# Kernel optimization log

Measured on AMD Instinct MI355X. Metric: run time of the kernel, lower is better.

## Reference

```python
import jax, jax.numpy as jnp
import numpy as np

E = 8            # n_expert
K = 2            # n_expert_per_token
C = 2048         # n_embd
I = 1408         # moe_intermediate_size
IS = I * 2       # shared expert intermediate (n_shared_expert=2)
B, T = 2, 2048


def setup_inputs() -> dict:
    key = jax.random.key(0)
    ks = jax.random.split(key, 9)
    s = 0.02
    return {
        "x": jax.random.normal(ks[0], (B, T, C), dtype=jnp.float32),
        "gate_w": jax.random.normal(ks[1], (E, C), dtype=jnp.float32) * s,
        # expert MLP weights, torch Linear convention (out_features, in_features)
        "w1": jax.random.normal(ks[2], (E, I, C), dtype=jnp.float32) * s,  # fc_1
        "w2": jax.random.normal(ks[3], (E, I, C), dtype=jnp.float32) * s,  # fc_2
        "w3": jax.random.normal(ks[4], (E, C, I), dtype=jnp.float32) * s,  # proj
        # shared expert
        "sw1": jax.random.normal(ks[5], (IS, C), dtype=jnp.float32) * s,
        "sw2": jax.random.normal(ks[6], (IS, C), dtype=jnp.float32) * s,
        "sw3": jax.random.normal(ks[7], (C, IS), dtype=jnp.float32) * s,
    }


def reference(x, gate_w, w1, w2, w3, sw1, sw2, sw3):
    Bq, Tq, Cq = x.shape
    xf = x.reshape(-1, Cq)  # [N, C], N = B*T

    # top-k routing: softmax in fp32, then top-k probs per token
    logits = xf @ gate_w.T                                   # [N, E]
    probs = jax.nn.softmax(logits.astype(jnp.float32), axis=-1)
    topk_p, topk_i = jax.lax.top_k(probs, K)                 # [N, K]
    # combine weights: comb[n, e] = sum_k topk_p[n,k] * (topk_i[n,k] == e)
    comb = (jax.nn.one_hot(topk_i, E, dtype=jnp.float32)
            * topk_p[..., None]).sum(axis=1).astype(x.dtype)  # [N, E]

    # per-expert gated-SiLU MLP (batched over experts via einsum)
    h1 = jnp.einsum('nc,eic->eni', xf, w1)                   # [E, N, I]
    h2 = jnp.einsum('nc,eic->eni', xf, w2)                   # [E, N, I]
    h = jax.nn.silu(h1) * h2
    eo = jnp.einsum('eni,eci->enc', h, w3)                   # [E, N, C]

    # weighted scatter-combine
    y = jnp.einsum('enc,ne->nc', eo, comb).reshape(Bq, Tq, Cq)

    # shared expert on the residual input
    sh = (jax.nn.silu(xf @ sw1.T) * (xf @ sw2.T)) @ sw3.T    # [N, C]
    return y + sh.reshape(Bq, Tq, Cq)
```

## Files before the change

### kernel.cpp

```cpp
#include <hip/hip_runtime.h>
#include <stdint.h>

#define N_TOK 4096
#define CDIM  2048
#define NEXP  8
#define IDIM  1408
#define ISDIM 2816
#define CAP   2048
#define ICAT  2816
#define SCAT  5632

typedef __attribute__((ext_vector_type(8))) short bf16x8;
typedef __attribute__((ext_vector_type(4))) float f32x4;

#define GLOAD16(gp, lp) __builtin_amdgcn_global_load_lds( \
    (const __attribute__((address_space(1))) void*)(gp),  \
    (__attribute__((address_space(3))) void*)(lp), 16, 0, 0)

__device__ __forceinline__ unsigned short f2bf(float f) {
  union { float f; unsigned u; } c; c.f = f;
  return (unsigned short)((c.u + 0x7FFFu + ((c.u >> 16) & 1u)) >> 16);
}
__device__ __forceinline__ float bf2f(unsigned short h) {
  union { unsigned u; float f; } c; c.u = (unsigned)h << 16;
  return c.f;
}

__global__ __launch_bounds__(256) void cvt_all(
    const float* __restrict__ x, const float* __restrict__ w1,
    const float* __restrict__ w2, const float* __restrict__ w3,
    const float* __restrict__ sw1, const float* __restrict__ sw2,
    const float* __restrict__ sw3,
    unsigned short* __restrict__ xb, unsigned short* __restrict__ wcat,
    unsigned short* __restrict__ w3b, unsigned short* __restrict__ swcat,
    unsigned short* __restrict__ sw3b) {
  const int b = blockIdx.x;
  const int t = threadIdx.x;
  const float* src;
  unsigned short* dst;
  if (b < 4096) {
    src = x + (size_t)b * 2048;  dst = xb + (size_t)b * 2048;
  } else if (b < 15360) {
    size_t o = (size_t)(b - 4096) * 2048;  src = w3 + o;  dst = w3b + o;
  } else if (b < 18176) {
    size_t o = (size_t)(b - 15360) * 2048; src = sw3 + o; dst = sw3b + o;
  } else if (b < 40704) {
    int g = b - 18176;
    int e = g / 2816, r = g - e * 2816;
    int dr;
    if (r < 1408) { src = w1 + ((size_t)e * 1408 + r) * 2048; dr = (r >> 7) * 256 + (r & 127); }
    else { int r2 = r - 1408; src = w2 + ((size_t)e * 1408 + r2) * 2048; dr = (r2 >> 7) * 256 + 128 + (r2 & 127); }
    dst = wcat + ((size_t)e * ICAT + dr) * 2048;
  } else {
    int g = b - 40704;
    int dr;
    if (g < 2816) {
      int zn = g >= 1408, rr = g - zn * 1408;
      src = sw1 + (size_t)g * 2048;
      dr = zn * 2816 + (rr >> 7) * 256 + (rr & 127);
    } else {
      int r = g - 2816;
      int zn = r >= 1408, rr = r - zn * 1408;
      src = sw2 + (size_t)r * 2048;
      dr = zn * 2816 + (rr >> 7) * 256 + 128 + (rr & 127);
    }
    dst = swcat + (size_t)dr * 2048;
  }
  size_t i = (size_t)t * 8;
  float4 v0 = *(const float4*)(src + i);
  float4 v1 = *(const float4*)(src + i + 4);
  bf16x8 o;
  o[0] = (short)f2bf(v0.x); o[1] = (short)f2bf(v0.y);
  o[2] = (short)f2bf(v0.z); o[3] = (short)f2bf(v0.w);
  o[4] = (short)f2bf(v1.x); o[5] = (short)f2bf(v1.y);
  o[6] = (short)f2bf(v1.z); o[7] = (short)f2bf(v1.w);
  *(bf16x8*)(dst + i) = o;
}

__global__ __launch_bounds__(64) void routing_kernel(
    const float* __restrict__ x, const float* __restrict__ gw,
    int* __restrict__ counts, int* __restrict__ list,
    int* __restrict__ slot_of, float* __restrict__ wts) {
  const int n = blockIdx.x;
  const int lane = threadIdx.x;
  const float* xr = x + (size_t)n * CDIM;
  float s[NEXP];
#pragma unroll
  for (int e = 0; e < NEXP; e++) s[e] = 0.f;
  for (int c = lane; c < CDIM; c += 64) {
    float xv = xr[c];
#pragma unroll
    for (int e = 0; e < NEXP; e++) s[e] += xv * gw[e * CDIM + c];
  }
#pragma unroll
  for (int e = 0; e < NEXP; e++) {
    float v = s[e];
    for (int o = 32; o > 0; o >>= 1) v += __shfl_down(v, o);
    s[e] = v;
  }
  if (lane == 0) {
    float mx = s[0];
#pragma unroll
    for (int e = 1; e < NEXP; e++) mx = fmaxf(mx, s[e]);
    float p[NEXP], sum = 0.f;
#pragma unroll
    for (int e = 0; e < NEXP; e++) { p[e] = __expf(s[e] - mx); sum += p[e]; }
    int i0 = 0;
#pragma unroll
    for (int e = 1; e < NEXP; e++) if (p[e] > p[i0]) i0 = e;
    int i1 = (i0 == 0) ? 1 : 0;
#pragma unroll
    for (int e = 0; e < NEXP; e++) if (e != i0 && p[e] > p[i1]) i1 = e;
    float inv = 1.f / sum;
    int s0 = atomicAdd(&counts[i0], 1);
    int s1 = atomicAdd(&counts[i1], 1);
    if (s0 < CAP) list[i0 * CAP + s0] = n; else s0 = 0;
    if (s1 < CAP) list[i1 * CAP + s1] = n; else s1 = 0;
    slot_of[n * 2]     = i0 * CAP + s0;
    slot_of[n * 2 + 1] = i1 * CAP + s1;
    wts[n * 2]     = p[i0] * inv;
    wts[n * 2 + 1] = p[i1] * inv;
  }
}

template <int PHASE>
__global__ __launch_bounds__(512) void moe_gemm(
    const unsigned short* __restrict__ xb,
    const unsigned short* __restrict__ swcat,
    const unsigned short* __restrict__ wcat,
    unsigned short* __restrict__ hs_out,
    unsigned short* __restrict__ he_out,
    const unsigned short* __restrict__ hs,
    const unsigned short* __restrict__ sw3b,
    const unsigned short* __restrict__ he,
    const unsigned short* __restrict__ w3b,
    float* __restrict__ ysf,
    unsigned short* __restrict__ eo,
    const int* __restrict__ list,
    const int* __restrict__ counts,
    int* __restrict__ ctr) {
  __shared__ __align__(16) char lds[3][32768];
  __shared__ int s_w;

  const int tid = threadIdx.x;
  const int srow = tid >> 2;
  const int c16  = (tid & 3) << 4;
  const int scol = c16 ^ (((srow >> 1) & 3) << 4);
  const int lane = tid & 63, wid = tid >> 6;
  const int wr = wid >> 2, wc = wid & 3;
  const int lrow = lane & 15;
  const int klane = (lane >> 4) << 4;
  const int rsw = ((lrow >> 1) & 3) << 4;
  const int aOff = (wr * 128 + lrow) * 64 + (klane ^ rsw);
  const int bOff = 16384 + (wc * 64 + lrow) * 64 + (klane ^ rsw);
  const int r4 = (lane >> 4) * 4;
  const int TOT = (PHASE == 1) ? 12 * 88 : 10 * 64;

  for (;;) {
    if (tid == 0) s_w = atomicAdd(ctr, 1);
    __syncthreads();
    const int w = s_w;
    if (w >= TOT) break;
    int z, mt, nt;
    if (PHASE == 1) { z = w / 88; int r = w - z * 88; mt = r & 7; nt = r >> 3; }
    else            { z = w / 64; int r = w - z * 64; mt = r & 7; nt = r >> 3; }

    const unsigned short *A, *B;
    unsigned short* O = nullptr;
    float* Of = nullptr;
    int Ka, ldo;
    int cnt = 1 << 30;
    const int* lst = nullptr;
    bool gath = false;
    if (PHASE == 1) {
      Ka = CDIM;
      if (z < 4) {
        int zm = z >> 1, zn = z & 1;
        A = xb + (size_t)zm * 2048 * CDIM;
        B = swcat + (size_t)zn * 2816 * CDIM;
        O = hs_out + (size_t)zm * 2048 * ISDIM + (size_t)zn * 1408;
        ldo = ISDIM;
      } else {
        int e = z - 4;
        cnt = counts[e]; if (cnt > CAP) cnt = CAP;
        lst = list + e * CAP;
        gath = true;
        A = xb;
        B = wcat + (size_t)e * ICAT * CDIM;
        O = he_out + (size_t)e * CAP * IDIM;
        ldo = IDIM;
      }
    } else {
      if (z < 2) {
        Ka = ISDIM;
        A = hs + (size_t)z * 2048 * ISDIM;
        B = sw3b;
        Of = ysf + (size_t)z * 2048 * CDIM;
        ldo = CDIM;
      } else {
        int e = z - 2;
        cnt = counts[e]; if (cnt > CAP) cnt = CAP;
        Ka = IDIM;
        A = he + (size_t)e * CAP * IDIM;
        B = w3b + (size_t)e * CDIM * IDIM;
        O = eo + (size_t)e * CAP * CDIM;
        ldo = CDIM;
      }
    }
    if (mt * 256 >= cnt) continue;

    const char *aS0, *aS1, *bS0, *bS1;
    {
      int ar0 = mt * 256 + srow;
      int ar1 = mt * 256 + 128 + srow;
      if (PHASE == 1 && gath) {
        ar0 = (ar0 < cnt) ? lst[ar0] : lst[0];
        ar1 = (ar1 < cnt) ? lst[ar1] : lst[0];
      }
      aS0 = (const char*)A + (size_t)ar0 * Ka * 2 + scol;
      aS1 = (const char*)A + (size_t)ar1 * Ka * 2 + scol;
      bS0 = (const char*)B + (size_t)(nt * 256 + srow) * Ka * 2 + scol;
      bS1 = (const char*)B + (size_t)(nt * 256 + 128 + srow) * Ka * 2 + scol;
    }
    auto stage = [&](int buf, int kt) {
      size_t kb = (size_t)kt * 64;
      char* d = &lds[buf][0] + tid * 16;
      GLOAD16(aS0 + kb, d);
      GLOAD16(aS1 + kb, d + 8192);
      GLOAD16(bS0 + kb, d + 16384);
      GLOAD16(bS1 + kb, d + 24576);
    };

    f32x4 acc[8][4];
#pragma unroll
    for (int mf = 0; mf < 8; mf++)
#pragma unroll
      for (int nf = 0; nf < 4; nf++) acc[mf][nf] = (f32x4){0.f, 0.f, 0.f, 0.f};

    stage(0, 0);
    stage(1, 1);

    const int ntk = Ka >> 5;
    int cur = 0, nx2 = 2;
    for (int t = 0; t < ntk; t++) {
      if (t + 1 < ntk) asm volatile("s_waitcnt vmcnt(4)" ::: "memory");
      else             asm volatile("s_waitcnt vmcnt(0)" ::: "memory");
      __builtin_amdgcn_s_barrier();
      const char* base = lds[cur];
      bf16x8 aR[8], bR[4];
#pragma unroll
      for (int i = 0; i < 8; i++) aR[i] = *(const bf16x8*)(base + aOff + i * 1024);
#pragma unroll
      for (int i = 0; i < 4; i++) bR[i] = *(const bf16x8*)(base + bOff + i * 1024);
      if (t + 2 < ntk) stage(nx2, t + 2);
      __builtin_amdgcn_s_setprio(1);
#pragma unroll
      for (int nf = 0; nf < 4; nf++)
#pragma unroll
        for (int mf = 0; mf < 8; mf++)
          acc[mf][nf] = __builtin_amdgcn_mfma_f32_16x16x32_bf16(
              aR[mf], bR[nf], acc[mf][nf], 0, 0, 0);
      __builtin_amdgcn_s_setprio(0);
      cur = (cur == 2) ? 0 : cur + 1;
      nx2 = (nx2 == 2) ? 0 : nx2 + 1;
    }

    if (PHASE == 1) {
      __syncthreads();
      unsigned short* ldsH = (unsigned short*)&lds[0][0];
      if (wc >= 2) {
        const int cb = (wc - 2) * 64;
#pragma unroll
        for (int mf = 0; mf < 8; mf++)
#pragma unroll
          for (int nf = 0; nf < 4; nf++) {
            int cc = cb + nf * 16 + lrow;
#pragma unroll
            for (int r = 0; r < 4; r++) {
              int rr = wr * 128 + mf * 16 + r4 + r;
              ldsH[rr * 128 + (cc ^ (((rr >> 2) & 7) << 4))] = f2bf(acc[mf][nf][r]);
            }
          }
      }
      __syncthreads();
      if (wc < 2) {
        const int cb = wc * 64;
#pragma unroll
        for (int mf = 0; mf < 8; mf++) {
#pragma unroll
          for (int nf = 0; nf < 4; nf++) {
            int cc = cb + nf * 16 + lrow;
            int col = nt * 128 + cc;
#pragma unroll
            for (int r = 0; r < 4; r++) {
              int rr = wr * 128 + mf * 16 + r4 + r;
              float z1 = acc[mf][nf][r];
              float z2 = bf2f(ldsH[rr * 128 + (cc ^ (((rr >> 2) & 7) << 4))]);
              float gv = z1 / (1.f + __expf(-z1)) * z2;
              O[(size_t)(mt * 256 + rr) * ldo + col] = f2bf(gv);
            }
          }
        }
      }
      __syncthreads();
    } else {
      const int rowb = mt * 256 + wr * 128;
      const int colb = nt * 256 + wc * 64;
#pragma unroll
      for (int mf = 0; mf < 8; mf++) {
        int row0 = rowb + mf * 16 + r4;
#pragma unroll
        for (int nf = 0; nf < 4; nf++) {
          int col = colb + nf * 16 + lrow;
#pragma unroll
          for (int r = 0; r < 4; r++) {
            if (z < 2)
              Of[(size_t)(row0 + r) * ldo + col] = acc[mf][nf][r];
            else
              O[(size_t)(row0 + r) * ldo + col] = f2bf(acc[mf][nf][r]);
          }
        }
      }
    }
  }
}

__global__ __launch_bounds__(256) void combine_kernel(
    float* __restrict__ y, const float* __restrict__ ysf,
    const unsigned short* __restrict__ eo,
    const int* __restrict__ slot_of, const float* __restrict__ wts) {
  int idx = blockIdx.x * 256 + threadIdx.x;
  int n = idx >> 9;
  int c = (idx & 511) * 4;
  float4 v = *(const float4*)(ysf + (size_t)n * CDIM + c);
#pragma unroll
  for (int k = 0; k < 2; k++) {
    int slot = slot_of[n * 2 + k];
    float w = wts[n * 2 + k];
    ushort4 h = *(const ushort4*)(eo + (size_t)slot * CDIM + c);
    v.x += w * bf2f(h.x);
    v.y += w * bf2f(h.y);
    v.z += w * bf2f(h.z);
    v.w += w * bf2f(h.w);
  }
  *(float4*)(y + (size_t)n * CDIM + c) = v;
}

extern "C" void kernel_launch(void* const* d_in, const int* in_sizes, int n_in,
                              void* d_out, int out_size, void* d_ws, size_t ws_size,
                              hipStream_t stream) {
  const float* x   = (const float*)d_in[0];
  const float* gw  = (const float*)d_in[1];
  const float* w1  = (const float*)d_in[2];
  const float* w2  = (const float*)d_in[3];
  const float* w3  = (const float*)d_in[4];
  const float* sw1 = (const float*)d_in[5];
  const float* sw2 = (const float*)d_in[6];
  const float* sw3 = (const float*)d_in[7];
  float* y = (float*)d_out;

  char* ws = (char*)d_ws;
  size_t off = 0;
  auto alloc = [&](size_t b) -> void* {
    void* p = ws + off;
    off += (b + 255) & ~(size_t)255;
    return p;
  };
  unsigned short* xb    = (unsigned short*)alloc((size_t)N_TOK * CDIM * 2);
  unsigned short* wcat  = (unsigned short*)alloc((size_t)NEXP * ICAT * CDIM * 2);
  unsigned short* w3b   = (unsigned short*)alloc((size_t)NEXP * CDIM * IDIM * 2);
  unsigned short* swcat = (unsigned short*)alloc((size_t)SCAT * CDIM * 2);
  unsigned short* sw3b  = (unsigned short*)alloc((size_t)CDIM * ISDIM * 2);
  unsigned short* hs    = (unsigned short*)alloc((size_t)N_TOK * ISDIM * 2);
  unsigned short* he    = (unsigned short*)alloc((size_t)NEXP * CAP * IDIM * 2);
  float*          ysf   = (float*)alloc((size_t)N_TOK * CDIM * 4);
  int*   counts  = (int*)alloc(NEXP * 4);
  int*   list    = (int*)alloc((size_t)NEXP * CAP * 4);
  int*   slot_of = (int*)alloc((size_t)N_TOK * 2 * 4);
  float* wtsb    = (float*)alloc((size_t)N_TOK * 2 * 4);
  int*   ctrs    = (int*)alloc(2 * 4);
  unsigned short* eoB = wcat;

  hipMemsetAsync(counts, 0, NEXP * 4, stream);
  hipMemsetAsync(ctrs, 0, 2 * 4, stream);
  routing_kernel<<<N_TOK, 64, 0, stream>>>(x, gw, counts, list, slot_of, wtsb);

  cvt_all<<<46336, 256, 0, stream>>>(x, w1, w2, w3, sw1, sw2, sw3,
                                     xb, wcat, w3b, swcat, sw3b);

  moe_gemm<1><<<dim3(256, 1, 1), 512, 0, stream>>>(
      xb, swcat, wcat, hs, he, hs, sw3b, he, w3b, ysf, eoB, list, counts, ctrs + 0);

  moe_gemm<2><<<dim3(256, 1, 1), 512, 0, stream>>>(
      xb, swcat, wcat, hs, he, hs, sw3b, he, w3b, ysf, eoB, list, counts, ctrs + 1);

  combine_kernel<<<(N_TOK * (CDIM / 4)) / 256, 256, 0, stream>>>(y, ysf, eoB, slot_of, wtsb);
}
```

Measured before the change: 596.0 us.

## Split shared-expert down-projection K dimension into two tiles with separate partial outputs

The shared-expert down-projection in phase 2 is split along its K dimension into two halves of 1408, doubling its tile count so the work items resemble the per-expert tiles (K=1408) and the persistent work queue balances better. Each half writes its own fp32 partial buffer, and the combine kernel sums the two partials. This adds an extra 32 MB fp32 buffer write and read in exchange for shorter, more even tail work in the GEMM.

```diff
diff --git a/kernel.cpp b/kernel.cpp
--- a/kernel.cpp
+++ b/kernel.cpp
@@ -134,7 +134,8 @@
     const unsigned short* __restrict__ sw3b,
     const unsigned short* __restrict__ he,
     const unsigned short* __restrict__ w3b,
-    float* __restrict__ ysf,
+    float* __restrict__ ysf0,
+    float* __restrict__ ysf1,
     unsigned short* __restrict__ eo,
     const int* __restrict__ list,
     const int* __restrict__ counts,
@@ -154,7 +155,7 @@
   const int aOff = (wr * 128 + lrow) * 64 + (klane ^ rsw);
   const int bOff = 16384 + (wc * 64 + lrow) * 64 + (klane ^ rsw);
   const int r4 = (lane >> 4) * 4;
-  const int TOT = (PHASE == 1) ? 12 * 88 : 10 * 64;
+  const int TOT = (PHASE == 1) ? 12 * 88 : 12 * 64;
 
   for (;;) {
     if (tid == 0) s_w = atomicAdd(ctr, 1);
@@ -163,17 +164,17 @@
     if (w >= TOT) break;
     int z, mt, nt;
     if (PHASE == 1) { z = w / 88; int r = w - z * 88; mt = r & 7; nt = r >> 3; }
-    else            { z = w / 64; int r = w - z * 64; mt = r & 7; nt = r >> 3; }
+    else            { z = w >> 6; int r = w & 63;     mt = r & 7; nt = r >> 3; }
 
     const unsigned short *A, *B;
     unsigned short* O = nullptr;
     float* Of = nullptr;
-    int Ka, ldo;
+    int Ka, lda, ldb, ldo;
     int cnt = 1 << 30;
     const int* lst = nullptr;
     bool gath = false;
     if (PHASE == 1) {
-      Ka = CDIM;
+      Ka = CDIM; lda = CDIM; ldb = CDIM;
       if (z < 4) {
         int zm = z >> 1, zn = z & 1;
         A = xb + (size_t)zm * 2048 * CDIM;
@@ -191,16 +192,18 @@
         ldo = IDIM;
       }
     } else {
-      if (z < 2) {
-        Ka = ISDIM;
-        A = hs + (size_t)z * 2048 * ISDIM;
-        B = sw3b;
-        Of = ysf + (size_t)z * 2048 * CDIM;
+      Ka = 1408;
+      if (z < 4) {
+        int zm = z >> 1, kh = z & 1;
+        lda = ISDIM; ldb = ISDIM;
+        A = hs + (size_t)zm * 2048 * ISDIM + (size_t)kh * 1408;
+        B = sw3b + (size_t)kh * 1408;
+        Of = (kh ? ysf1 : ysf0) + (size_t)zm * 2048 * CDIM;
         ldo = CDIM;
       } else {
-        int e = z - 2;
+        int e = z - 4;
         cnt = counts[e]; if (cnt > CAP) cnt = CAP;
-        Ka = IDIM;
+        lda = IDIM; ldb = IDIM;
         A = he + (size_t)e * CAP * IDIM;
         B = w3b + (size_t)e * CDIM * IDIM;
         O = eo + (size_t)e * CAP * CDIM;
@@ -217,10 +220,10 @@
         ar0 = (ar0 < cnt) ? lst[ar0] : lst[0];
         ar1 = (ar1 < cnt) ? lst[ar1] : lst[0];
       }
-      aS0 = (const char*)A + (size_t)ar0 * Ka * 2 + scol;
-      aS1 = (const char*)A + (size_t)ar1 * Ka * 2 + scol;
-      bS0 = (const char*)B + (size_t)(nt * 256 + srow) * Ka * 2 + scol;
-      bS1 = (const char*)B + (size_t)(nt * 256 + 128 + srow) * Ka * 2 + scol;
+      aS0 = (const char*)A + (size_t)ar0 * lda * 2 + scol;
+      aS1 = (const char*)A + (size_t)ar1 * lda * 2 + scol;
+      bS0 = (const char*)B + (size_t)(nt * 256 + srow) * ldb * 2 + scol;
+      bS1 = (const char*)B + (size_t)(nt * 256 + 128 + srow) * ldb * 2 + scol;
     }
     auto stage = [&](int buf, int kt) {
       size_t kb = (size_t)kt * 64;
@@ -314,7 +317,7 @@
           int col = colb + nf * 16 + lrow;
 #pragma unroll
           for (int r = 0; r < 4; r++) {
-            if (z < 2)
+            if (z < 4)
               Of[(size_t)(row0 + r) * ldo + col] = acc[mf][nf][r];
             else
               O[(size_t)(row0 + r) * ldo + col] = f2bf(acc[mf][nf][r]);
@@ -326,13 +329,16 @@
 }
 
 __global__ __launch_bounds__(256) void combine_kernel(
-    float* __restrict__ y, const float* __restrict__ ysf,
+    float* __restrict__ y, const float* __restrict__ ysf0,
+    const float* __restrict__ ysf1,
     const unsigned short* __restrict__ eo,
     const int* __restrict__ slot_of, const float* __restrict__ wts) {
   int idx = blockIdx.x * 256 + threadIdx.x;
   int n = idx >> 9;
   int c = (idx & 511) * 4;
-  float4 v = *(const float4*)(ysf + (size_t)n * CDIM + c);
+  float4 v = *(const float4*)(ysf0 + (size_t)n * CDIM + c);
+  float4 v1 = *(const float4*)(ysf1 + (size_t)n * CDIM + c);
+  v.x += v1.x; v.y += v1.y; v.z += v1.z; v.w += v1.w;
 #pragma unroll
   for (int k = 0; k < 2; k++) {
     int slot = slot_of[n * 2 + k];
@@ -373,7 +379,8 @@
   unsigned short* sw3b  = (unsigned short*)alloc((size_t)CDIM * ISDIM * 2);
   unsigned short* hs    = (unsigned short*)alloc((size_t)N_TOK * ISDIM * 2);
   unsigned short* he    = (unsigned short*)alloc((size_t)NEXP * CAP * IDIM * 2);
-  float*          ysf   = (float*)alloc((size_t)N_TOK * CDIM * 4);
+  float*          ysf0  = (float*)alloc((size_t)N_TOK * CDIM * 4);
+  float*          ysf1  = (float*)alloc((size_t)N_TOK * CDIM * 4);
   int*   counts  = (int*)alloc(NEXP * 4);
   int*   list    = (int*)alloc((size_t)NEXP * CAP * 4);
   int*   slot_of = (int*)alloc((size_t)N_TOK * 2 * 4);
@@ -389,10 +396,13 @@
                                      xb, wcat, w3b, swcat, sw3b);
 
   moe_gemm<1><<<dim3(256, 1, 1), 512, 0, stream>>>(
-      xb, swcat, wcat, hs, he, hs, sw3b, he, w3b, ysf, eoB, list, counts, ctrs + 0);
+      xb, swcat, wcat, hs, he, hs, sw3b, he, w3b, ysf0, ysf1, eoB,
+      list, counts, ctrs + 0);
 
   moe_gemm<2><<<dim3(256, 1, 1), 512, 0, stream>>>(
-      xb, swcat, wcat, hs, he, hs, sw3b, he, w3b, ysf, eoB, list, counts, ctrs + 1);
-
-  combine_kernel<<<(N_TOK * (CDIM / 4)) / 256, 256, 0, stream>>>(y, ysf, eoB, slot_of, wtsb);
-}
+      xb, swcat, wcat, hs, he, hs, sw3b, he, w3b, ysf0, ysf1, eoB,
+      list, counts, ctrs + 1);
+
+  combine_kernel<<<(N_TOK * (CDIM / 4)) / 256, 256, 0, stream>>>(
+      y, ysf0, ysf1, eoB, slot_of, wtsb);
+}
```

Result: slower. 618.7 us (+3.8%).

## Partition GEMM work queue into per-XCD panel segments for cache locality

Applied to the files above, without the earlier changes.

Replaces the single global atomic work counter with eight per-segment counters. Each block starts on the segment selected by its blockIdx modulo 8 and steals from the other segments once its own is drained. Panels (z, nt) are interleaved across segments so that blocks on the same XCD tend to process all M-tiles of one weight panel, with the intent of reusing B tiles in that XCD's L2. Costs include extra counters and the possibility of contention or imbalance toward the end of the work.

```diff
diff --git a/kernel.cpp b/kernel.cpp
--- a/kernel.cpp
+++ b/kernel.cpp
@@ -154,170 +154,176 @@
   const int aOff = (wr * 128 + lrow) * 64 + (klane ^ rsw);
   const int bOff = 16384 + (wc * 64 + lrow) * 64 + (klane ^ rsw);
   const int r4 = (lane >> 4) * 4;
-  const int TOT = (PHASE == 1) ? 12 * 88 : 10 * 64;
-
-  for (;;) {
-    if (tid == 0) s_w = atomicAdd(ctr, 1);
-    __syncthreads();
-    const int w = s_w;
-    if (w >= TOT) break;
-    int z, mt, nt;
-    if (PHASE == 1) { z = w / 88; int r = w - z * 88; mt = r & 7; nt = r >> 3; }
-    else            { z = w / 64; int r = w - z * 64; mt = r & 7; nt = r >> 3; }
-
-    const unsigned short *A, *B;
-    unsigned short* O = nullptr;
-    float* Of = nullptr;
-    int Ka, ldo;
-    int cnt = 1 << 30;
-    const int* lst = nullptr;
-    bool gath = false;
-    if (PHASE == 1) {
-      Ka = CDIM;
-      if (z < 4) {
-        int zm = z >> 1, zn = z & 1;
-        A = xb + (size_t)zm * 2048 * CDIM;
-        B = swcat + (size_t)zn * 2816 * CDIM;
-        O = hs_out + (size_t)zm * 2048 * ISDIM + (size_t)zn * 1408;
-        ldo = ISDIM;
+  const int NPAN = (PHASE == 1) ? 132 : 80;
+  const int NTD  = (PHASE == 1) ? 11 : 8;
+  const int myseg = blockIdx.x & 7;
+
+  for (int soff = 0; soff < 8; soff++) {
+    const int seg = (myseg + soff) & 7;
+    const int cap = (((NPAN - seg + 7) >> 3) << 3);
+    for (;;) {
+      if (tid == 0) s_w = atomicAdd(&ctr[seg], 1);
+      __syncthreads();
+      const int i = s_w;
+      if (i >= cap) break;
+      const int panel = seg + ((i >> 3) << 3);
+      const int mt = i & 7;
+      const int z = panel / NTD, nt = panel % NTD;
+
+      const unsigned short *A, *B;
+      unsigned short* O = nullptr;
+      float* Of = nullptr;
+      int Ka, ldo;
+      int cnt = 1 << 30;
+      const int* lst = nullptr;
+      bool gath = false;
+      if (PHASE == 1) {
+        Ka = CDIM;
+        if (z < 4) {
+          int zm = z >> 1, zn = z & 1;
+          A = xb + (size_t)zm * 2048 * CDIM;
+          B = swcat + (size_t)zn * 2816 * CDIM;
+          O = hs_out + (size_t)zm * 2048 * ISDIM + (size_t)zn * 1408;
+          ldo = ISDIM;
+        } else {
+          int e = z - 4;
+          cnt = counts[e]; if (cnt > CAP) cnt = CAP;
+          lst = list + e * CAP;
+          gath = true;
+          A = xb;
+          B = wcat + (size_t)e * ICAT * CDIM;
+          O = he_out + (size_t)e * CAP * IDIM;
+          ldo = IDIM;
+        }
       } else {
-        int e = z - 4;
-        cnt = counts[e]; if (cnt > CAP) cnt = CAP;
-        lst = list + e * CAP;
-        gath = true;
-        A = xb;
-        B = wcat + (size_t)e * ICAT * CDIM;
-        O = he_out + (size_t)e * CAP * IDIM;
-        ldo = IDIM;
+        if (z < 2) {
+          Ka = ISDIM;
+          A = hs + (size_t)z * 2048 * ISDIM;
+          B = sw3b;
+          Of = ysf + (size_t)z * 2048 * CDIM;
+          ldo = CDIM;
+        } else {
+          int e = z - 2;
+          cnt = counts[e]; if (cnt > CAP) cnt = CAP;
+          Ka = IDIM;
+          A = he + (size_t)e * CAP * IDIM;
+          B = w3b + (size_t)e * CDIM * IDIM;
+          O = eo + (size_t)e * CAP * CDIM;
+          ldo = CDIM;
+        }
       }
-    } else {
-      if (z < 2) {
-        Ka = ISDIM;
-        A = hs + (size_t)z * 2048 * ISDIM;
-        B = sw3b;
-        Of = ysf + (size_t)z * 2048 * CDIM;
-        ldo = CDIM;
-      } else {
-        int e = z - 2;
-        cnt = counts[e]; if (cnt > CAP) cnt = CAP;
-        Ka = IDIM;
-        A = he + (size_t)e * CAP * IDIM;
-        B = w3b + (size_t)e * CDIM * IDIM;
-        O = eo + (size_t)e * CAP * CDIM;
-        ldo = CDIM;
+      if (mt * 256 >= cnt) continue;
+
+      const char *aS0, *aS1, *bS0, *bS1;
+      {
+        int ar0 = mt * 256 + srow;
+        int ar1 = mt * 256 + 128 + srow;
+        if (PHASE == 1 && gath) {
+          ar0 = (ar0 < cnt) ? lst[ar0] : lst[0];
+          ar1 = (ar1 < cnt) ? lst[ar1] : lst[0];
+        }
+        aS0 = (const char*)A + (size_t)ar0 * Ka * 2 + scol;
+        aS1 = (const char*)A + (size_t)ar1 * Ka * 2 + scol;
+        bS0 = (const char*)B + (size_t)(nt * 256 + srow) * Ka * 2 + scol;
+        bS1 = (const char*)B + (size_t)(nt * 256 + 128 + srow) * Ka * 2 + scol;
       }
-    }
-    if (mt * 256 >= cnt) continue;
-
-    const char *aS0, *aS1, *bS0, *bS1;
-    {
-      int ar0 = mt * 256 + srow;
-      int ar1 = mt * 256 + 128 + srow;
-      if (PHASE == 1 && gath) {
-        ar0 = (ar0 < cnt) ? lst[ar0] : lst[0];
-        ar1 = (ar1 < cnt) ? lst[ar1] : lst[0];
+      auto stage = [&](int buf, int kt) {
+        size_t kb = (size_t)kt * 64;
+        char* d = &lds[buf][0] + tid * 16;
+        GLOAD16(aS0 + kb, d);
+        GLOAD16(aS1 + kb, d + 8192);
+        GLOAD16(bS0 + kb, d + 16384);
+        GLOAD16(bS1 + kb, d + 24576);
+      };
+
+      f32x4 acc[8][4];
+#pragma unroll
+      for (int mf = 0; mf < 8; mf++)
+#pragma unroll
+        for (int nf = 0; nf < 4; nf++) acc[mf][nf] = (f32x4){0.f, 0.f, 0.f, 0.f};
+
+      stage(0, 0);
+      stage(1, 1);
+
+      const int ntk = Ka >> 5;
+      int cur = 0, nx2 = 2;
+      for (int t = 0; t < ntk; t++) {
+        if (t + 1 < ntk) asm volatile("s_waitcnt vmcnt(4)" ::: "memory");
+        else             asm volatile("s_waitcnt vmcnt(0)" ::: "memory");
+        __builtin_amdgcn_s_barrier();
+        const char* base = lds[cur];
+        bf16x8 aR[8], bR[4];
+#pragma unroll
+        for (int i2 = 0; i2 < 8; i2++) aR[i2] = *(const bf16x8*)(base + aOff + i2 * 1024);
+#pragma unroll
+        for (int i2 = 0; i2 < 4; i2++) bR[i2] = *(const bf16x8*)(base + bOff + i2 * 1024);
+        if (t + 2 < ntk) stage(nx2, t + 2);
+        __builtin_amdgcn_s_setprio(1);
+#pragma unroll
+        for (int nf = 0; nf < 4; nf++)
+#pragma unroll
+          for (int mf = 0; mf < 8; mf++)
+            acc[mf][nf] = __builtin_amdgcn_mfma_f32_16x16x32_bf16(
+                aR[mf], bR[nf], acc[mf][nf], 0, 0, 0);
+        __builtin_amdgcn_s_setprio(0);
+        cur = (cur == 2) ? 0 : cur + 1;
+        nx2 = (nx2 == 2) ? 0 : nx2 + 1;
       }
-      aS0 = (const char*)A + (size_t)ar0 * Ka * 2 + scol;
-      aS1 = (const char*)A + (size_t)ar1 * Ka * 2 + scol;
-      bS0 = (const char*)B + (size_t)(nt * 256 + srow) * Ka * 2 + scol;
-      bS1 = (const char*)B + (size_t)(nt * 256 + 128 + srow) * Ka * 2 + scol;
-    }
-    auto stage = [&](int buf, int kt) {
-      size_t kb = (size_t)kt * 64;
-      char* d = &lds[buf][0] + tid * 16;
-      GLOAD16(aS0 + kb, d);
-      GLOAD16(aS1 + kb, d + 8192);
-      GLOAD16(bS0 + kb, d + 16384);
-      GLOAD16(bS1 + kb, d + 24576);
-    };
-
-    f32x4 acc[8][4];
-#pragma unroll
-    for (int mf = 0; mf < 8; mf++)
-#pragma unroll
-      for (int nf = 0; nf < 4; nf++) acc[mf][nf] = (f32x4){0.f, 0.f, 0.f, 0.f};
-
-    stage(0, 0);
-    stage(1, 1);
-
-    const int ntk = Ka >> 5;
-    int cur = 0, nx2 = 2;
-    for (int t = 0; t < ntk; t++) {
-      if (t + 1 < ntk) asm volatile("s_waitcnt vmcnt(4)" ::: "memory");
-      else             asm volatile("s_waitcnt vmcnt(0)" ::: "memory");
-      __builtin_amdgcn_s_barrier();
-      const char* base = lds[cur];
-      bf16x8 aR[8], bR[4];
-#pragma unroll
-      for (int i = 0; i < 8; i++) aR[i] = *(const bf16x8*)(base + aOff + i * 1024);
-#pragma unroll
-      for (int i = 0; i < 4; i++) bR[i] = *(const bf16x8*)(base + bOff + i * 1024);
-      if (t + 2 < ntk) stage(nx2, t + 2);
-      __builtin_amdgcn_s_setprio(1);
-#pragma unroll
-      for (int nf = 0; nf < 4; nf++)
-#pragma unroll
-        for (int mf = 0; mf < 8; mf++)
-          acc[mf][nf] = __builtin_amdgcn_mfma_f32_16x16x32_bf16(
-              aR[mf], bR[nf], acc[mf][nf], 0, 0, 0);
-      __builtin_amdgcn_s_setprio(0);
-      cur = (cur == 2) ? 0 : cur + 1;
-      nx2 = (nx2 == 2) ? 0 : nx2 + 1;
-    }
-
-    if (PHASE == 1) {
-      __syncthreads();
-      unsigned short* ldsH = (unsigned short*)&lds[0][0];
-      if (wc >= 2) {
-        const int cb = (wc - 2) * 64;
-#pragma unroll
-        for (int mf = 0; mf < 8; mf++)
-#pragma unroll
-          for (int nf = 0; nf < 4; nf++) {
-            int cc = cb + nf * 16 + lrow;
-#pragma unroll
-            for (int r = 0; r < 4; r++) {
-              int rr = wr * 128 + mf * 16 + r4 + r;
-              ldsH[rr * 128 + (cc ^ (((rr >> 2) & 7) << 4))] = f2bf(acc[mf][nf][r]);
+
+      if (PHASE == 1) {
+        __syncthreads();
+        unsigned short* ldsH = (unsigned short*)&lds[0][0];
+        if (wc >= 2) {
+          const int cb = (wc - 2) * 64;
+#pragma unroll
+          for (int mf = 0; mf < 8; mf++)
+#pragma unroll
+            for (int nf = 0; nf < 4; nf++) {
+              int cc = cb + nf * 16 + lrow;
+#pragma unroll
+              for (int r = 0; r < 4; r++) {
+                int rr = wr * 128 + mf * 16 + r4 + r;
+                ldsH[rr * 128 + (cc ^ (((rr >> 2) & 7) << 4))] = f2bf(acc[mf][nf][r]);
+              }
+            }
+        }
+        __syncthreads();
+        if (wc < 2) {
+          const int cb = wc * 64;
+#pragma unroll
+          for (int mf = 0; mf < 8; mf++) {
+#pragma unroll
+            for (int nf = 0; nf < 4; nf++) {
+              int cc = cb + nf * 16 + lrow;
+              int col = nt * 128 + cc;
+#pragma unroll
+              for (int r = 0; r < 4; r++) {
+                int rr = wr * 128 + mf * 16 + r4 + r;
+                float z1 = acc[mf][nf][r];
+                float z2 = bf2f(ldsH[rr * 128 + (cc ^ (((rr >> 2) & 7) << 4))]);
+                float gv = z1 / (1.f + __expf(-z1)) * z2;
+                O[(size_t)(mt * 256 + rr) * ldo + col] = f2bf(gv);
+              }
             }
           }
-      }
-      __syncthreads();
-      if (wc < 2) {
-        const int cb = wc * 64;
+        }
+        __syncthreads();
+      } else {
+        const int rowb = mt * 256 + wr * 128;
+        const int colb = nt * 256 + wc * 64;
 #pragma unroll
         for (int mf = 0; mf < 8; mf++) {
+          int row0 = rowb + mf * 16 + r4;
 #pragma unroll
           for (int nf = 0; nf < 4; nf++) {
-            int cc = cb + nf * 16 + lrow;
-            int col = nt * 128 + cc;
+            int col = colb + nf * 16 + lrow;
 #pragma unroll
             for (int r = 0; r < 4; r++) {
-              int rr = wr * 128 + mf * 16 + r4 + r;
-              float z1 = acc[mf][nf][r];
-              float z2 = bf2f(ldsH[rr * 128 + (cc ^ (((rr >> 2) & 7) << 4))]);
-              float gv = z1 / (1.f + __expf(-z1)) * z2;
-              O[(size_t)(mt * 256 + rr) * ldo + col] = f2bf(gv);
+              if (z < 2)
+                Of[(size_t)(row0 + r) * ldo + col] = acc[mf][nf][r];
+              else
+                O[(size_t)(row0 + r) * ldo + col] = f2bf(acc[mf][nf][r]);
             }
-          }
-        }
-      }
-      __syncthreads();
-    } else {
-      const int rowb = mt * 256 + wr * 128;
-      const int colb = nt * 256 + wc * 64;
-#pragma unroll
-      for (int mf = 0; mf < 8; mf++) {
-        int row0 = rowb + mf * 16 + r4;
-#pragma unroll
-        for (int nf = 0; nf < 4; nf++) {
-          int col = colb + nf * 16 + lrow;
-#pragma unroll
-          for (int r = 0; r < 4; r++) {
-            if (z < 2)
-              Of[(size_t)(row0 + r) * ldo + col] = acc[mf][nf][r];
-            else
-              O[(size_t)(row0 + r) * ldo + col] = f2bf(acc[mf][nf][r]);
           }
         }
       }
@@ -378,21 +384,24 @@
   int*   list    = (int*)alloc((size_t)NEXP * CAP * 4);
   int*   slot_of = (int*)alloc((size_t)N_TOK * 2 * 4);
   float* wtsb    = (float*)alloc((size_t)N_TOK * 2 * 4);
-  int*   ctrs    = (int*)alloc(2 * 4);
+  int*   ctrs    = (int*)alloc(16 * 4);
   unsigned short* eoB = wcat;
 
   hipMemsetAsync(counts, 0, NEXP * 4, stream);
-  hipMemsetAsync(ctrs, 0, 2 * 4, stream);
+  hipMemsetAsync(ctrs, 0, 16 * 4, stream);
   routing_kernel<<<N_TOK, 64, 0, stream>>>(x, gw, counts, list, slot_of, wtsb);
 
   cvt_all<<<46336, 256, 0, stream>>>(x, w1, w2, w3, sw1, sw2, sw3,
                                      xb, wcat, w3b, swcat, sw3b);
 
   moe_gemm<1><<<dim3(256, 1, 1), 512, 0, stream>>>(
-      xb, swcat, wcat, hs, he, hs, sw3b, he, w3b, ysf, eoB, list, counts, ctrs + 0);
+      xb, swcat, wcat, hs, he, hs, sw3b, he, w3b, ysf, eoB,
+      list, counts, ctrs + 0);
 
   moe_gemm<2><<<dim3(256, 1, 1), 512, 0, stream>>>(
-      xb, swcat, wcat, hs, he, hs, sw3b, he, w3b, ysf, eoB, list, counts, ctrs + 1);
-
-  combine_kernel<<<(N_TOK * (CDIM / 4)) / 256, 256, 0, stream>>>(y, ysf, eoB, slot_of, wtsb);
-}
+      xb, swcat, wcat, hs, he, hs, sw3b, he, w3b, ysf, eoB,
+      list, counts, ctrs + 8);
+
+  combine_kernel<<<(N_TOK * (CDIM / 4)) / 256, 256, 0, stream>>>(
+      y, ysf, eoB, slot_of, wtsb);
+}
```

New measurement: 626.7 us. 5.1% more time.
